# Optimization experiments

Hardware: AMD Instinct MI355X
Metric: run time of the kernel (lower is better)

## Reference

```python
import jax, jax.numpy as jnp
import numpy as np

B, T, V, H, M = 32, 40, 64, 768, 64
U = 23            # number of never-visited vpids
N = 63            # total distinct vpids: visited 0..T-1, unvisited T..N-1
POS_D = 7         # angle_feat_size(4) + 3
MAX_STEPS = 100
TXT_L = 60
LN_EPS = 1e-12


def setup_inputs() -> dict:
    key = jax.random.key(0)
    ks = jax.random.split(key, 12)
    split_traj_embeds = jax.random.normal(ks[0], (B, T, V, H), jnp.float32)
    split_traj_vp_lens = jax.random.randint(ks[1], (B, T), 1, V + 1)
    traj_vpids = jnp.broadcast_to(jnp.arange(T, dtype=jnp.int32), (B, T))
    cand = jax.random.randint(ks[2], (B, T, V), 0, N).astype(jnp.int32)
    # guarantee every unvisited vpid (T..N-1) appears as a candidate at step 0
    cand = cand.at[:, 0, :U].set(jnp.broadcast_to(T + jnp.arange(U, dtype=jnp.int32), (B, U)))
    # gmap node 0 is the 'stop' token (feature forced to zero); nodes 1.. list all vpids
    gmap_vpids = jnp.broadcast_to(
        jnp.concatenate([jnp.zeros((1,), jnp.int32), jnp.arange(N, dtype=jnp.int32)]), (B, M))
    gmap_step_ids = jax.random.randint(ks[3], (B, M), 0, MAX_STEPS).astype(jnp.int32)
    gmap_pos_fts = jax.random.normal(ks[4], (B, M, POS_D), jnp.float32)
    gmap_lens = jax.random.randint(ks[5], (B,), M // 2, M + 1).astype(jnp.int32)
    txt_embeds = jax.random.normal(ks[6], (B, TXT_L, H), jnp.float32)
    txt_masks = jnp.ones((B, TXT_L), bool)
    # learned params
    W_pos = jax.random.normal(ks[7], (POS_D, H), jnp.float32) / np.sqrt(POS_D)
    b_pos = jnp.zeros((H,), jnp.float32)
    ln_gamma = jnp.ones((H,), jnp.float32)
    ln_beta = jnp.zeros((H,), jnp.float32)
    step_table = jax.random.normal(ks[8], (MAX_STEPS, H), jnp.float32) * 0.02
    return {
        'txt_embeds': txt_embeds, 'txt_masks': txt_masks,
        'split_traj_embeds': split_traj_embeds, 'split_traj_vp_lens': split_traj_vp_lens,
        'traj_vpids': traj_vpids, 'traj_cand_vpids': cand, 'gmap_vpids': gmap_vpids,
        'gmap_step_ids': gmap_step_ids, 'gmap_pos_fts': gmap_pos_fts, 'gmap_lens': gmap_lens,
        'W_pos': W_pos, 'b_pos': b_pos, 'ln_gamma': ln_gamma, 'ln_beta': ln_beta,
        'step_table': step_table,
    }


def _aggregate(split_traj_embeds, vp_lens, traj_vpids, traj_cand_vpids, gmap_vpids):
    dt = split_traj_embeds.dtype
    # mask out padded views, like split_traj_embeds * vp_masks
    view_mask = (jnp.arange(V) < vp_lens[:, :, None]).astype(dt)        # [B,T,V]
    emb_masked = split_traj_embeds * view_mask[..., None]               # [B,T,V,H]
    # per-step visited feature: sum over views / vp_len
    step_mean = emb_masked.sum(axis=2) / vp_lens[..., None].astype(dt)  # [B,T,H]
    # visited lookup: last step t with traj_vpids == gmap vpid
    visit_match = gmap_vpids[:, :, None] == traj_vpids[:, None, :]      # [B,M,T]
    visited = jnp.any(visit_match, axis=-1)                             # [B,M]
    last_t = jnp.argmax(jnp.where(visit_match, jnp.arange(T), -1), axis=-1)  # [B,M]
    visited_feat = step_mean[jnp.arange(B)[:, None], last_t]            # [B,M,H]
    # unvisited: mean of candidate-slot features over all (t, j) matches
    cand_match = (gmap_vpids[:, :, None, None] == traj_cand_vpids[:, None, :, :]).astype(dt)  # [B,M,T,V]
    unvis_sum = jnp.einsum('bmtv,btvh->bmh', cand_match, emb_masked)
    cnt = cand_match.sum(axis=(2, 3))                                   # [B,M]
    unvis_feat = unvis_sum / jnp.maximum(cnt, 1.0)[..., None]
    agg = jnp.where(visited[..., None], visited_feat, unvis_feat)       # [B,M,H]
    return agg.at[:, 0, :].set(0.0)  # stop-token slot is zeros


def _layernorm(x, gamma, beta):
    mu = x.mean(axis=-1, keepdims=True)
    var = ((x - mu) ** 2).mean(axis=-1, keepdims=True)
    return (x - mu) * jax.lax.rsqrt(var + LN_EPS) * gamma + beta


def reference(txt_embeds, txt_masks, split_traj_embeds, split_traj_vp_lens, traj_vpids,
              traj_cand_vpids, gmap_vpids, gmap_step_ids, gmap_pos_fts, gmap_lens,
              W_pos, b_pos, ln_gamma, ln_beta, step_table):
    agg = _aggregate(split_traj_embeds, split_traj_vp_lens, traj_vpids,
                     traj_cand_vpids, gmap_vpids)
    pos = _layernorm(gmap_pos_fts @ W_pos + b_pos, ln_gamma, ln_beta)   # [B,M,H]
    step = step_table[gmap_step_ids]                                    # [B,M,H]
    gmap_embeds = agg + step + pos
    return gmap_embeds
```

## Files before the change

kernel.cpp:

```cpp
#include <hip/hip_runtime.h>
#include <cstdint>

#define B 32
#define T 40
#define V 64
#define H 768
#define M 64
#define POS_D 7
#define NCODE 64
#define NBINS 32
#define NBIN_BLKS (B * NBINS)
#define CH 16
#define NCHK 4
#define NSTEPC (B * T * NCHK)
#define SEG 32

__global__ __launch_bounds__(192) void k1_kernel(
    const float* __restrict__ emb, const int* __restrict__ lens,
    const int* __restrict__ cand, const int* __restrict__ tvp,
    const int* __restrict__ gvp,
    float* __restrict__ part,
    float* __restrict__ Sdiv)
{
    const int tid = threadIdx.x;

    if (blockIdx.x >= NBIN_BLKS) {
        const int idx = blockIdx.x - NBIN_BLKS;
        const int bt = idx >> 2, c = idx & 3;
        const int len = lens[bt];
        const int v0 = c * CH;
        if (v0 >= len) return;
        const float* base = emb + ((size_t)bt * V + v0) * H + tid * 4;
        float ax = 0.f, ay = 0.f, az = 0.f, aw = 0.f;
        if (v0 + CH <= len) {
            #pragma unroll
            for (int v = 0; v < CH; ++v) {
                const float4 x = *(const float4*)(base + (size_t)v * H);
                ax += x.x; ay += x.y; az += x.z; aw += x.w;
            }
        } else {
            const int n = len - v0;
            #pragma unroll 4
            for (int v = 0; v < n; ++v) {
                const float4 x = *(const float4*)(base + (size_t)v * H);
                ax += x.x; ay += x.y; az += x.z; aw += x.w;
            }
        }
        const float inv = 1.0f / (float)len;
        float4 o; o.x = ax * inv; o.y = ay * inv; o.z = az * inv; o.w = aw * inv;
        *(float4*)(part + (size_t)idx * H + tid * 4) = o;
        return;
    }

    const int bb = blockIdx.x;
    const int b = bb >> 5, bin = bb & 31;
    const int w = tid >> 6, lane = tid & 63;

    __shared__ int tvp_s[T], gvp_s[M], lens_s[T];
    __shared__ int code_s, cnt_s;
    __shared__ int list_s[3 * SEG];
    __shared__ int wcnt[3];

    if (tid < T) { tvp_s[tid] = tvp[b * T + tid]; lens_s[tid] = lens[b * T + tid]; }
    if (tid < M) gvp_s[tid] = gvp[b * M + tid];
    if (tid == 0) { code_s = -1; cnt_s = 0; }
    if (tid < 3) wcnt[tid] = 0;
    __syncthreads();

    if (tid < 64) {
        const int c = tid;
        bool mention = false;
        #pragma unroll 8
        for (int mm = 0; mm < M; ++mm) mention |= (gvp_s[mm] == c);
        bool vis = false;
        #pragma unroll 8
        for (int t = 0; t < T; ++t) vis |= (tvp_s[t] == c);
        const bool needed = mention && !vis;
        const unsigned long long mask = __ballot(needed);
        const int pre = __popcll(mask & ((1ull << c) - 1ull));
        if (needed && pre == bin) code_s = c;
    }
    __syncthreads();

    const int code = code_s;
    float ax = 0.f, ay = 0.f, az = 0.f, aw = 0.f;
    if (code >= 0) {
        const int* cb = cand + b * T * V;
        int local = 0;
        for (int i = tid; i < T * V; i += 192) local += (cb[i] == code);
        #pragma unroll
        for (int off = 32; off; off >>= 1) local += __shfl_xor(local, off);
        if (lane == 0) atomicAdd(&cnt_s, local);

        int myn = 0;
        for (int t = w; t < T; t += 3) {
            const int cc = cb[t * V + lane];
            const bool ok = (lane < lens_s[t]) && (cc == code);
            const unsigned long long mk = __ballot(ok);
            if (ok) {
                const int pos = myn + __popcll(mk & ((1ull << lane) - 1ull));
                if (pos < SEG) list_s[w * SEG + pos] = t * V + lane;
            }
            myn += __popcll(mk);
        }
        if (lane == 0) wcnt[w] = min(myn, SEG);
    }
    __syncthreads();

    if (code >= 0) {
        const float* eb = emb + (size_t)b * T * V * H + tid * 4;
        for (int ww = 0; ww < 3; ++ww) {
            const int n = wcnt[ww];
            #pragma unroll 8
            for (int k = 0; k < n; ++k) {
                const int tvx = list_s[ww * SEG + k];
                const float4 x = *(const float4*)(eb + (size_t)tvx * H);
                ax += x.x; ay += x.y; az += x.z; aw += x.w;
            }
        }
        const float inv = 1.0f / fmaxf((float)cnt_s, 1.0f);
        ax *= inv; ay *= inv; az *= inv; aw *= inv;
    }
    float4 o; o.x = ax; o.y = ay; o.z = az; o.w = aw;
    *(float4*)(Sdiv + (size_t)bb * H + tid * 4) = o;
}

__global__ __launch_bounds__(192) void k2_kernel(
    const int* __restrict__ gvp, const int* __restrict__ tvp,
    const int* __restrict__ lens, const int* __restrict__ step_ids,
    const float* __restrict__ pos_fts, const float* __restrict__ part,
    const float* __restrict__ Sdiv, const float* __restrict__ W_pos,
    const float* __restrict__ b_pos, const float* __restrict__ gamma,
    const float* __restrict__ beta, const float* __restrict__ step_tab,
    float* __restrict__ out)
{
    const int bm = blockIdx.x;
    const int b = bm >> 6;
    const int m = bm & 63;
    const int tid = threadIdx.x;
    const int hl = tid * 4;

    __shared__ int tvp_s[T], gvp_s[M];
    __shared__ unsigned long long needmask;
    if (tid < T) tvp_s[tid] = tvp[b * T + tid];
    if (tid < M) gvp_s[tid] = gvp[b * M + tid];
    __syncthreads();
    if (tid < 64) {
        const int c = tid;
        bool mention = false;
        #pragma unroll 8
        for (int mm = 0; mm < M; ++mm) mention |= (gvp_s[mm] == c);
        bool vis = false;
        #pragma unroll 8
        for (int t = 0; t < T; ++t) vis |= (tvp_s[t] == c);
        const unsigned long long mask = __ballot(mention && !vis);
        if (tid == 0) needmask = mask;
    }
    __syncthreads();

    const int g = gvp_s[m];
    float ax = 0.f, ay = 0.f, az = 0.f, aw = 0.f;
    if (m != 0 && g >= 0 && g < NCODE) {
        int lt = -1;
        #pragma unroll 8
        for (int t = 0; t < T; ++t) if (tvp_s[t] == g) lt = t;
        if (lt >= 0) {
            const int len = lens[b * T + lt];
            const int nch = (len + CH - 1) / CH;
            for (int i = 0; i < nch; ++i) {
                const float4 x = *(const float4*)(
                    part + ((size_t)(b * T + lt) * NCHK + i) * H + hl);
                ax += x.x; ay += x.y; az += x.z; aw += x.w;
            }
        } else if ((needmask >> g) & 1ull) {
            const int bin = __popcll(needmask & ((1ull << g) - 1ull));
            if (bin < NBINS) {
                const float4 s = *(const float4*)(
                    Sdiv + ((size_t)b * NBINS + bin) * H + hl);
                ax = s.x; ay = s.y; az = s.z; aw = s.w;
            }
        }
    }

    float f[POS_D];
    #pragma unroll
    for (int d = 0; d < POS_D; ++d) f[d] = pos_fts[bm * POS_D + d];
    const float4 bp = *(const float4*)(b_pos + hl);
    float px = bp.x, py = bp.y, pz = bp.z, pw = bp.w;
    #pragma unroll
    for (int d = 0; d < POS_D; ++d) {
        const float4 wv4 = *(const float4*)(W_pos + d * H + hl);
        px += f[d] * wv4.x; py += f[d] * wv4.y; pz += f[d] * wv4.z; pw += f[d] * wv4.w;
    }

    float s1 = px + py + pz + pw;
    float s2 = px * px + py * py + pz * pz + pw * pw;
    #pragma unroll
    for (int off = 32; off > 0; off >>= 1) {
        s1 += __shfl_xor(s1, off);
        s2 += __shfl_xor(s2, off);
    }
    __shared__ float w1[3], w2[3];
    const int wv = tid >> 6;
    if ((tid & 63) == 0) { w1[wv] = s1; w2[wv] = s2; }
    __syncthreads();
    s1 = w1[0] + w1[1] + w1[2];
    s2 = w2[0] + w2[1] + w2[2];
    const float mu = s1 * (1.0f / H);
    const float var = fmaxf(s2 * (1.0f / H) - mu * mu, 0.f);
    const float rs = rsqrtf(var + 1e-12f);

    const float4 gm = *(const float4*)(gamma + hl);
    const float4 bt = *(const float4*)(beta + hl);
    const int sid = step_ids[bm];
    const float4 st = *(const float4*)(step_tab + (size_t)sid * H + hl);

    float4 o;
    o.x = ax + st.x + (px - mu) * rs * gm.x + bt.x;
    o.y = ay + st.y + (py - mu) * rs * gm.y + bt.y;
    o.z = az + st.z + (pz - mu) * rs * gm.z + bt.z;
    o.w = aw + st.w + (pw - mu) * rs * gm.w + bt.w;
    *(float4*)(out + (size_t)bm * H + hl) = o;
}

extern "C" void kernel_launch(void* const* d_in, const int* in_sizes, int n_in,
                              void* d_out, int out_size, void* d_ws, size_t ws_size,
                              hipStream_t stream)
{
    const float* emb      = (const float*)d_in[2];
    const int*   vp_lens  = (const int*)d_in[3];
    const int*   tvp      = (const int*)d_in[4];
    const int*   cand     = (const int*)d_in[5];
    const int*   gvp      = (const int*)d_in[6];
    const int*   step_ids = (const int*)d_in[7];
    const float* pos_fts  = (const float*)d_in[8];
    const float* W_pos    = (const float*)d_in[10];
    const float* b_pos    = (const float*)d_in[11];
    const float* gamma    = (const float*)d_in[12];
    const float* beta     = (const float*)d_in[13];
    const float* step_tab = (const float*)d_in[14];
    float* out = (float*)d_out;

    char* ws = (char*)d_ws;
    size_t off = 0;
    float* part = (float*)(ws + off); off += (size_t)NSTEPC * H * sizeof(float);
    float* Sdiv = (float*)(ws + off); off += (size_t)B * NBINS * H * sizeof(float);

    k1_kernel<<<NBIN_BLKS + NSTEPC, 192, 0, stream>>>(emb, vp_lens, cand, tvp, gvp,
                                                      part, Sdiv);
    k2_kernel<<<B * M, 192, 0, stream>>>(gvp, tvp, vp_lens, step_ids, pos_fts,
                                         part, Sdiv, W_pos, b_pos, gamma, beta,
                                         step_tab, out);
}
```

Before: 49.54 us.

## Replace chunked step-mean blocks with persistent atomic work queue in k1

The k1 kernel no longer launches a separate block per (step, 16-row chunk). It launches one block per (batch, bin); each block first computes its unvisited-vpid mean and then pulls whole steps from a global atomic counter, averaging all valid rows into a per-step mean. k2 now reads a single precomputed step mean instead of summing up to four partial chunks. This aims to cut block launch overhead and partial-sum traffic and to balance load dynamically. The cost is a memset plus one atomic and two barriers per step item, with only 1024 blocks streaming the large embedding tensor.

```diff
diff --git a/kernel.cpp b/kernel.cpp
--- a/kernel.cpp
+++ b/kernel.cpp
@@ -9,130 +9,129 @@
 #define POS_D 7
 #define NCODE 64
 #define NBINS 32
-#define NBIN_BLKS (B * NBINS)
-#define CH 16
-#define NCHK 4
-#define NSTEPC (B * T * NCHK)
+#define NBLK (B * NBINS)
+#define NSTEP (B * T)
 #define SEG 32
 
-__global__ __launch_bounds__(192) void k1_kernel(
+__global__ __launch_bounds__(192, 3) void k1_kernel(
     const float* __restrict__ emb, const int* __restrict__ lens,
     const int* __restrict__ cand, const int* __restrict__ tvp,
     const int* __restrict__ gvp,
-    float* __restrict__ part,
-    float* __restrict__ Sdiv)
+    float* __restrict__ step_mean,
+    float* __restrict__ Sdiv,
+    unsigned int* __restrict__ ctr)
 {
     const int tid = threadIdx.x;
-
-    if (blockIdx.x >= NBIN_BLKS) {
-        const int idx = blockIdx.x - NBIN_BLKS;
-        const int bt = idx >> 2, c = idx & 3;
-        const int len = lens[bt];
-        const int v0 = c * CH;
-        if (v0 >= len) return;
-        const float* base = emb + ((size_t)bt * V + v0) * H + tid * 4;
+    const int w = tid >> 6, lane = tid & 63;
+
+    {
+        const int bb = blockIdx.x;
+        const int b = bb >> 5, bin = bb & 31;
+
+        __shared__ int tvp_s[T], gvp_s[M], lens_s[T];
+        __shared__ int code_s, cnt_s;
+        __shared__ int list_s[3 * SEG];
+        __shared__ int wcnt[3];
+
+        if (tid < T) { tvp_s[tid] = tvp[b * T + tid]; lens_s[tid] = lens[b * T + tid]; }
+        if (tid < M) gvp_s[tid] = gvp[b * M + tid];
+        if (tid == 0) { code_s = -1; cnt_s = 0; }
+        if (tid < 3) wcnt[tid] = 0;
+        __syncthreads();
+
+        if (tid < 64) {
+            const int c = tid;
+            bool mention = false;
+            #pragma unroll 8
+            for (int mm = 0; mm < M; ++mm) mention |= (gvp_s[mm] == c);
+            bool vis = false;
+            #pragma unroll 8
+            for (int t = 0; t < T; ++t) vis |= (tvp_s[t] == c);
+            const bool needed = mention && !vis;
+            const unsigned long long mask = __ballot(needed);
+            const int pre = __popcll(mask & ((1ull << c) - 1ull));
+            if (needed && pre == bin) code_s = c;
+        }
+        __syncthreads();
+
+        const int code = code_s;
         float ax = 0.f, ay = 0.f, az = 0.f, aw = 0.f;
-        if (v0 + CH <= len) {
+        if (code >= 0) {
+            const int* cb = cand + b * T * V;
+            int local = 0;
+            for (int i = tid; i < T * V; i += 192) local += (cb[i] == code);
             #pragma unroll
-            for (int v = 0; v < CH; ++v) {
-                const float4 x = *(const float4*)(base + (size_t)v * H);
+            for (int off = 32; off; off >>= 1) local += __shfl_xor(local, off);
+            if (lane == 0) atomicAdd(&cnt_s, local);
+
+            int myn = 0;
+            for (int t = w; t < T; t += 3) {
+                const int cc = cb[t * V + lane];
+                const bool ok = (lane < lens_s[t]) && (cc == code);
+                const unsigned long long mk = __ballot(ok);
+                if (ok) {
+                    const int pos = myn + __popcll(mk & ((1ull << lane) - 1ull));
+                    if (pos < SEG) list_s[w * SEG + pos] = t * V + lane;
+                }
+                myn += __popcll(mk);
+            }
+            if (lane == 0) wcnt[w] = min(myn, SEG);
+            __syncthreads();
+
+            const float* eb = emb + (size_t)b * T * V * H + tid * 4;
+            for (int ww = 0; ww < 3; ++ww) {
+                const int n = wcnt[ww];
+                #pragma unroll 8
+                for (int k = 0; k < n; ++k) {
+                    const int tvx = list_s[ww * SEG + k];
+                    const float4 x = *(const float4*)(eb + (size_t)tvx * H);
+                    ax += x.x; ay += x.y; az += x.z; aw += x.w;
+                }
+            }
+            const float inv = 1.0f / fmaxf((float)cnt_s, 1.0f);
+            ax *= inv; ay *= inv; az *= inv; aw *= inv;
+        }
+        float4 o; o.x = ax; o.y = ay; o.z = az; o.w = aw;
+        *(float4*)(Sdiv + (size_t)bb * H + tid * 4) = o;
+    }
+
+    __shared__ int item_s;
+    for (;;) {
+        __syncthreads();
+        if (tid == 0) item_s = (int)atomicAdd(ctr, 1u);
+        __syncthreads();
+        const int it = item_s;
+        if (it >= NSTEP) break;
+
+        const int len = lens[it];
+        const float* base = emb + (size_t)it * V * H + tid * 4;
+        float ax = 0.f, ay = 0.f, az = 0.f, aw = 0.f;
+        int v = 0;
+        for (; v + 16 <= len; v += 16) {
+            #pragma unroll
+            for (int u = 0; u < 16; ++u) {
+                const float4 x = *(const float4*)(base + (size_t)(v + u) * H);
                 ax += x.x; ay += x.y; az += x.z; aw += x.w;
             }
-        } else {
-            const int n = len - v0;
-            #pragma unroll 4
-            for (int v = 0; v < n; ++v) {
-                const float4 x = *(const float4*)(base + (size_t)v * H);
-                ax += x.x; ay += x.y; az += x.z; aw += x.w;
-            }
+        }
+        #pragma unroll 4
+        for (; v < len; ++v) {
+            const float4 x = *(const float4*)(base + (size_t)v * H);
+            ax += x.x; ay += x.y; az += x.z; aw += x.w;
         }
         const float inv = 1.0f / (float)len;
         float4 o; o.x = ax * inv; o.y = ay * inv; o.z = az * inv; o.w = aw * inv;
-        *(float4*)(part + (size_t)idx * H + tid * 4) = o;
-        return;
-    }
-
-    const int bb = blockIdx.x;
-    const int b = bb >> 5, bin = bb & 31;
-    const int w = tid >> 6, lane = tid & 63;
-
-    __shared__ int tvp_s[T], gvp_s[M], lens_s[T];
-    __shared__ int code_s, cnt_s;
-    __shared__ int list_s[3 * SEG];
-    __shared__ int wcnt[3];
-
-    if (tid < T) { tvp_s[tid] = tvp[b * T + tid]; lens_s[tid] = lens[b * T + tid]; }
-    if (tid < M) gvp_s[tid] = gvp[b * M + tid];
-    if (tid == 0) { code_s = -1; cnt_s = 0; }
-    if (tid < 3) wcnt[tid] = 0;
-    __syncthreads();
-
-    if (tid < 64) {
-        const int c = tid;
-        bool mention = false;
-        #pragma unroll 8
-        for (int mm = 0; mm < M; ++mm) mention |= (gvp_s[mm] == c);
-        bool vis = false;
-        #pragma unroll 8
-        for (int t = 0; t < T; ++t) vis |= (tvp_s[t] == c);
-        const bool needed = mention && !vis;
-        const unsigned long long mask = __ballot(needed);
-        const int pre = __popcll(mask & ((1ull << c) - 1ull));
-        if (needed && pre == bin) code_s = c;
-    }
-    __syncthreads();
-
-    const int code = code_s;
-    float ax = 0.f, ay = 0.f, az = 0.f, aw = 0.f;
-    if (code >= 0) {
-        const int* cb = cand + b * T * V;
-        int local = 0;
-        for (int i = tid; i < T * V; i += 192) local += (cb[i] == code);
-        #pragma unroll
-        for (int off = 32; off; off >>= 1) local += __shfl_xor(local, off);
-        if (lane == 0) atomicAdd(&cnt_s, local);
-
-        int myn = 0;
-        for (int t = w; t < T; t += 3) {
-            const int cc = cb[t * V + lane];
-            const bool ok = (lane < lens_s[t]) && (cc == code);
-            const unsigned long long mk = __ballot(ok);
-            if (ok) {
-                const int pos = myn + __popcll(mk & ((1ull << lane) - 1ull));
-                if (pos < SEG) list_s[w * SEG + pos] = t * V + lane;
-            }
-            myn += __popcll(mk);
-        }
-        if (lane == 0) wcnt[w] = min(myn, SEG);
-    }
-    __syncthreads();
-
-    if (code >= 0) {
-        const float* eb = emb + (size_t)b * T * V * H + tid * 4;
-        for (int ww = 0; ww < 3; ++ww) {
-            const int n = wcnt[ww];
-            #pragma unroll 8
-            for (int k = 0; k < n; ++k) {
-                const int tvx = list_s[ww * SEG + k];
-                const float4 x = *(const float4*)(eb + (size_t)tvx * H);
-                ax += x.x; ay += x.y; az += x.z; aw += x.w;
-            }
-        }
-        const float inv = 1.0f / fmaxf((float)cnt_s, 1.0f);
-        ax *= inv; ay *= inv; az *= inv; aw *= inv;
-    }
-    float4 o; o.x = ax; o.y = ay; o.z = az; o.w = aw;
-    *(float4*)(Sdiv + (size_t)bb * H + tid * 4) = o;
+        *(float4*)(step_mean + (size_t)it * H + tid * 4) = o;
+    }
 }
 
 __global__ __launch_bounds__(192) void k2_kernel(
     const int* __restrict__ gvp, const int* __restrict__ tvp,
-    const int* __restrict__ lens, const int* __restrict__ step_ids,
-    const float* __restrict__ pos_fts, const float* __restrict__ part,
-    const float* __restrict__ Sdiv, const float* __restrict__ W_pos,
-    const float* __restrict__ b_pos, const float* __restrict__ gamma,
-    const float* __restrict__ beta, const float* __restrict__ step_tab,
-    float* __restrict__ out)
+    const int* __restrict__ step_ids, const float* __restrict__ pos_fts,
+    const float* __restrict__ step_mean, const float* __restrict__ Sdiv,
+    const float* __restrict__ W_pos, const float* __restrict__ b_pos,
+    const float* __restrict__ gamma, const float* __restrict__ beta,
+    const float* __restrict__ step_tab, float* __restrict__ out)
 {
     const int bm = blockIdx.x;
     const int b = bm >> 6;
@@ -165,13 +164,9 @@
         #pragma unroll 8
         for (int t = 0; t < T; ++t) if (tvp_s[t] == g) lt = t;
         if (lt >= 0) {
-            const int len = lens[b * T + lt];
-            const int nch = (len + CH - 1) / CH;
-            for (int i = 0; i < nch; ++i) {
-                const float4 x = *(const float4*)(
-                    part + ((size_t)(b * T + lt) * NCHK + i) * H + hl);
-                ax += x.x; ay += x.y; az += x.z; aw += x.w;
-            }
+            const float4 sm = *(const float4*)(
+                step_mean + ((size_t)b * T + lt) * H + hl);
+            ax = sm.x; ay = sm.y; az = sm.z; aw = sm.w;
         } else if ((needmask >> g) & 1ull) {
             const int bin = __popcll(needmask & ((1ull << g) - 1ull));
             if (bin < NBINS) {
@@ -243,12 +238,14 @@
 
     char* ws = (char*)d_ws;
     size_t off = 0;
-    float* part = (float*)(ws + off); off += (size_t)NSTEPC * H * sizeof(float);
-    float* Sdiv = (float*)(ws + off); off += (size_t)B * NBINS * H * sizeof(float);
-
-    k1_kernel<<<NBIN_BLKS + NSTEPC, 192, 0, stream>>>(emb, vp_lens, cand, tvp, gvp,
-                                                      part, Sdiv);
-    k2_kernel<<<B * M, 192, 0, stream>>>(gvp, tvp, vp_lens, step_ids, pos_fts,
-                                         part, Sdiv, W_pos, b_pos, gamma, beta,
-                                         step_tab, out);
+    float* step_mean = (float*)(ws + off); off += (size_t)NSTEP * H * sizeof(float);
+    float* Sdiv      = (float*)(ws + off); off += (size_t)B * NBINS * H * sizeof(float);
+    unsigned int* ctr = (unsigned int*)(ws + off); off += 256;
+
+    hipMemsetAsync(ctr, 0, sizeof(unsigned int), stream);
+    k1_kernel<<<NBLK, 192, 0, stream>>>(emb, vp_lens, cand, tvp, gvp,
+                                        step_mean, Sdiv, ctr);
+    k2_kernel<<<B * M, 192, 0, stream>>>(gvp, tvp, step_ids, pos_fts,
+                                         step_mean, Sdiv, W_pos, b_pos,
+                                         gamma, beta, step_tab, out);
 }
```

New measurement: 57.68 us. +16.4%, slower.
